# Kernel tuning notes

Hardware: AMD Instinct MI355X
Metric: run time of the kernel (lower is better)

The kernel has to match this reference:

```python
import jax, jax.numpy as jnp
import numpy as np

N = 50000      # nodes
E = 1600000    # edges (avg degree 32)
D = 64         # in_features
OUT = 64       # out_features


def setup_inputs() -> dict:
    key = jax.random.key(0)
    ks = jax.random.split(key, 6)
    x = jax.random.normal(ks[0], (N, D), jnp.float32)
    h0 = jax.random.normal(ks[1], (N, D), jnp.float32)
    edge_row = jax.random.randint(ks[2], (E,), 0, N, jnp.int32)
    edge_col = jax.random.randint(ks[3], (E,), 0, N, jnp.int32)
    edge_vals = jax.random.uniform(ks[4], (E,), jnp.float32)  # normalized adj values
    stdv = 1.0 / np.sqrt(OUT)
    W = jax.random.uniform(ks[5], (D, OUT), jnp.float32, -stdv, stdv)
    lamda = jnp.full((1,), 0.5, jnp.float32)
    s = jnp.full((1,), 0.1, jnp.float32)  # alpha in GCNII
    l = 4  # layer index
    return {"x": x, "h0": h0, "edge_vals": edge_vals, "W": W,
            "edge_row": edge_row, "edge_col": edge_col,
            "lamda": lamda, "s": s, "l": l}


def reference(x, h0, edge_vals, W, edge_row, edge_col, lamda, s, l):
    # theta = lamda / l
    theta = lamda / jnp.float32(l)  # [1]
    # hi = spmm(adj, x): COO gather-scale-scatter
    msgs = edge_vals[:, None] * x[edge_col]            # [E, D]
    hi = jax.ops.segment_sum(msgs, edge_row, num_segments=N)  # [N, D]
    # useAOR=True, variant=False: support = (1-s)*hi + s*h0; r = support
    support = (1.0 - s) * hi + s * h0                  # [N, D]
    # useDLR=True: output = theta * support @ W + (1-theta) * support
    output = theta * (support @ W) + (1.0 - theta) * support  # [N, OUT]
    # residual=False
    return output
```

## Files before the change

### kernel.cpp

```cpp
#include <hip/hip_runtime.h>

#define NN 50000
#define NE 1600000
#define DD 64
#define RB 128
#define NBK 391
#define BINS 512
#define EPB 4096
#define NBLKA 391
#define CAP 6144
#define G4 800000
#define CONVB 196

__device__ __forceinline__ unsigned f2bf(float f) {
    unsigned u = __float_as_uint(f);
    u += 0x7FFFu + ((u >> 16) & 1u);
    return (u >> 16) & 0xFFFFu;
}

__global__ __launch_bounds__(1024) void scatter_conv(
    const int* __restrict__ erow, const int* __restrict__ ecol,
    const float* __restrict__ evals, const float* __restrict__ x,
    uint2* __restrict__ xb, int* __restrict__ gcur,
    unsigned* __restrict__ pkv, unsigned char* __restrict__ rlb)
{
    int tid = threadIdx.x;
    if (blockIdx.x >= NBLKA) {
        int t = (blockIdx.x - NBLKA) * 1024 + tid;
        const float4* x4 = reinterpret_cast<const float4*>(x);
        #pragma unroll
        for (int i = 0; i < 4; ++i) {
            int g = i * (CONVB * 1024) + t;
            if (g < G4) {
                float4 v = x4[g];
                uint2 o;
                o.x = f2bf(v.x) | (f2bf(v.y) << 16);
                o.y = f2bf(v.z) | (f2bf(v.w) << 16);
                xb[g] = o;
            }
        }
        return;
    }

    __shared__ int hist[BINS];
    __shared__ int lstart[BINS];
    __shared__ int gbase[BINS];
    __shared__ unsigned datap[EPB];
    __shared__ unsigned char datarl[EPB];
    __shared__ unsigned short sbkt[EPB];

    if (tid < BINS) hist[tid] = 0;
    __syncthreads();

    int base = blockIdx.x * EPB;
    int r[4], c[4], bk[4]; float v[4];
    #pragma unroll
    for (int i = 0; i < 4; ++i) {
        int e = base + i * 1024 + tid;
        if (e < NE) {
            r[i] = erow[e]; c[i] = ecol[e]; v[i] = evals[e];
            bk[i] = r[i] >> 7;
            atomicAdd(&hist[bk[i]], 1);
        } else bk[i] = -1;
    }
    __syncthreads();

    if (tid < 64) {
        int cc[8], s = 0;
        #pragma unroll
        for (int i = 0; i < 8; ++i) { cc[i] = hist[tid * 8 + i]; s += cc[i]; }
        int vv = s;
        #pragma unroll
        for (int off = 1; off < 64; off <<= 1) {
            int u = __shfl_up(vv, off, 64);
            if (tid >= off) vv += u;
        }
        int run = vv - s;
        #pragma unroll
        for (int i = 0; i < 8; ++i) { lstart[tid * 8 + i] = run; run += cc[i]; }
    }
    __syncthreads();

    if (tid < BINS) {
        int cnt = hist[tid];
        gbase[tid] = cnt ? atomicAdd(&gcur[tid], cnt) : 0;
        hist[tid] = lstart[tid];
    }
    __syncthreads();

    #pragma unroll
    for (int i = 0; i < 4; ++i) {
        if (bk[i] >= 0) {
            int p = atomicAdd(&hist[bk[i]], 1);
            datap[p]  = (f2bf(v[i]) << 16) | (unsigned)c[i];
            datarl[p] = (unsigned char)(r[i] & (RB - 1));
            sbkt[p]   = (unsigned short)bk[i];
        }
    }
    __syncthreads();

    int total = NE - base; if (total > EPB) total = EPB;
    #pragma unroll
    for (int i = 0; i < 4; ++i) {
        int slot = i * 1024 + tid;
        if (slot < total) {
            int bb = sbkt[slot];
            int dst = bb * CAP + gbase[bb] + slot - lstart[bb];
            pkv[dst] = datap[slot];
            rlb[dst] = datarl[slot];
        }
    }
}

__global__ __launch_bounds__(1024) void row_sort(
    const int* __restrict__ gcur, unsigned* pkv,
    const unsigned char* __restrict__ rlb, int2* __restrict__ rs)
{
    __shared__ int rhist[RB];
    __shared__ int rstart[RB + 1];

    int tid = threadIdx.x;
    int b = blockIdx.x;
    int base = b * CAP;
    int count = gcur[b];

    if (tid < RB) rhist[tid] = 0;
    __syncthreads();

    unsigned av[CAP / 1024];
    int rl[CAP / 1024];
    #pragma unroll
    for (int i = 0; i < CAP / 1024; ++i) {
        int idx = i * 1024 + tid;
        if (idx < count) {
            av[i] = pkv[base + idx];
            rl[i] = rlb[base + idx];
            atomicAdd(&rhist[rl[i]], 1);
        } else rl[i] = -1;
    }
    __syncthreads();

    if (tid < 64) {
        int pc0 = (rhist[tid * 2] + 7) & ~7;
        int pc1 = (rhist[tid * 2 + 1] + 7) & ~7;
        int ssum = pc0 + pc1, vv = ssum;
        #pragma unroll
        for (int off = 1; off < 64; off <<= 1) {
            int u = __shfl_up(vv, off, 64);
            if (tid >= off) vv += u;
        }
        int run = vv - ssum;
        rstart[tid * 2]     = run;
        rstart[tid * 2 + 1] = run + pc0;
        if (tid == 63) rstart[RB] = run + pc0 + pc1;
    }
    __syncthreads();

    if (tid < RB) {
        int rr = b * RB + tid;
        if (rr < NN)
            rs[rr] = make_int2(base + rstart[tid], rstart[tid + 1] - rstart[tid]);
        rhist[tid] = rstart[tid];
    }
    __syncthreads();

    int p[CAP / 1024];
    #pragma unroll
    for (int i = 0; i < CAP / 1024; ++i)
        if (rl[i] >= 0) p[i] = atomicAdd(&rhist[rl[i]], 1);
    __syncthreads();

    #pragma unroll
    for (int i = 0; i < CAP / 1024; ++i)
        if (rl[i] >= 0) pkv[base + p[i]] = av[i];
    if (tid < RB)
        for (int idx = rhist[tid]; idx < rstart[tid + 1]; ++idx)
            pkv[base + idx] = 0;
}

__global__ __launch_bounds__(256, 4) void spmm_gemm(
    const uint2* __restrict__ xb, const float* __restrict__ h0,
    const float* __restrict__ W,  const float* __restrict__ lamda,
    const float* __restrict__ s_ptr, const int* __restrict__ l_ptr,
    const int2* __restrict__ rs, const unsigned* __restrict__ pkv,
    float* __restrict__ out)
{
    __shared__ float Wp[DD * DD];

    float theta = lamda[0] / (float)l_ptr[0];
    float s     = s_ptr[0];

    for (int i = threadIdx.x; i < DD * DD; i += 256) {
        int k = i >> 6, j = i & 63;
        float wv = theta * W[i];
        if (k == j) wv += (1.0f - theta);
        Wp[i] = wv;
    }
    __syncthreads();

    int tid    = threadIdx.x;
    int f4     = tid & 15;
    int parity = (tid >> 4) & 1;
    int gb     = tid & 48;
    int r      = blockIdx.x * 8 + (tid >> 5);

    int2 se = rs[r];
    int end = se.x + se.y;

    float4 acc = make_float4(0.f, 0.f, 0.f, 0.f);

    #define FMA1(U, Q)                                                      \
        {                                                                   \
            float vv = __uint_as_float((U) & 0xFFFF0000u);                  \
            acc.x = fmaf(vv, __uint_as_float((Q).x << 16), acc.x);          \
            acc.y = fmaf(vv, __uint_as_float((Q).x & 0xFFFF0000u), acc.y);  \
            acc.z = fmaf(vv, __uint_as_float((Q).y << 16), acc.z);          \
            acc.w = fmaf(vv, __uint_as_float((Q).y & 0xFFFF0000u), acc.w);  \
        }

    int e = se.x + parity * 8;
    unsigned myu = (e < end) ? pkv[e + (f4 & 7)] : 0;
    for (; e < end; e += 16) {
        unsigned nxt = (e + 16 < end) ? pkv[e + 16 + (f4 & 7)] : 0;
        unsigned u[8]; uint2 q[8];
        #pragma unroll
        for (int j = 0; j < 8; ++j) u[j] = __shfl(myu, gb + j, 64);
        #pragma unroll
        for (int j = 0; j < 8; ++j)
            q[j] = xb[(size_t)(u[j] & 0xFFFFu) * 16 + f4];
        #pragma unroll
        for (int j = 0; j < 8; ++j) FMA1(u[j], q[j]);
        myu = nxt;
    }
    #undef FMA1

    acc.x += __shfl_xor(acc.x, 16, 64);
    acc.y += __shfl_xor(acc.y, 16, 64);
    acc.z += __shfl_xor(acc.z, 16, 64);
    acc.w += __shfl_xor(acc.w, 16, 64);

    float4 hb = *reinterpret_cast<const float4*>(h0 + (size_t)r * DD + f4 * 4);
    float oms = 1.0f - s;
    float4 sup;
    sup.x = oms * acc.x + s * hb.x;
    sup.y = oms * acc.y + s * hb.y;
    sup.z = oms * acc.z + s * hb.z;
    sup.w = oms * acc.w + s * hb.w;

    float4 o = make_float4(0.f, 0.f, 0.f, 0.f);
    #pragma unroll
    for (int kk = 0; kk < 32; ++kk) {
        int k = parity * 32 + kk;
        float comp = ((kk & 3) == 0) ? sup.x :
                     ((kk & 3) == 1) ? sup.y :
                     ((kk & 3) == 2) ? sup.z : sup.w;
        float sk = __shfl(comp, gb + parity * 8 + (kk >> 2), 64);
        float4 w = *reinterpret_cast<const float4*>(&Wp[k * DD + f4 * 4]);
        o.x = fmaf(sk, w.x, o.x);
        o.y = fmaf(sk, w.y, o.y);
        o.z = fmaf(sk, w.z, o.z);
        o.w = fmaf(sk, w.w, o.w);
    }
    o.x += __shfl_xor(o.x, 16, 64);
    o.y += __shfl_xor(o.y, 16, 64);
    o.z += __shfl_xor(o.z, 16, 64);
    o.w += __shfl_xor(o.w, 16, 64);

    if (parity == 0)
        *reinterpret_cast<float4*>(out + (size_t)r * DD + f4 * 4) = o;
}

extern "C" void kernel_launch(void* const* d_in, const int* in_sizes, int n_in,
                              void* d_out, int out_size, void* d_ws, size_t ws_size,
                              hipStream_t stream) {
    const float* x     = (const float*)d_in[0];
    const float* h0    = (const float*)d_in[1];
    const float* evals = (const float*)d_in[2];
    const float* W     = (const float*)d_in[3];
    const int*   erow  = (const int*)d_in[4];
    const int*   ecol  = (const int*)d_in[5];
    const float* lamda = (const float*)d_in[6];
    const float* s_ptr = (const float*)d_in[7];
    const int*   l_ptr = (const int*)d_in[8];
    float* out = (float*)d_out;

    char* ws = (char*)d_ws;
    int*           gcur = (int*)ws;
    int2*          rs   = (int2*)(ws + 2048);
    size_t         pkv_off = 2048 + (((size_t)NN * 8 + 255) & ~(size_t)255);
    unsigned*      pkv  = (unsigned*)(ws + pkv_off);
    uint2*         xb   = (uint2*)(ws + pkv_off + (size_t)NBK * CAP * 4);
    unsigned char* rlb  = (unsigned char*)(ws + pkv_off + (size_t)NBK * CAP * 4
                                              + (size_t)NN * DD * 2);

    hipMemsetAsync(gcur, 0, 2048, stream);

    scatter_conv<<<NBLKA + CONVB, 1024, 0, stream>>>(erow, ecol, evals, x, xb,
                                                     gcur, pkv, rlb);
    row_sort    <<<NBK, 1024, 0, stream>>>(gcur, pkv, rlb, rs);
    spmm_gemm   <<<NN / 8, 256, 0, stream>>>(xb, h0, W, lamda, s_ptr, l_ptr,
                                             rs, pkv, out);
}
```

Baseline: 72.24 us.

## Fuse row-bucket sort into SpMM+GEMM kernel using shared-memory sorted edges

Merges the row_sort and spmm_gemm kernels into one. Each block sorts a 64-row bucket's edges into shared memory and then computes the SpMM and the dense transform for those rows directly from LDS. Bucket size shrinks from 128 to 64 rows (782 buckets, capacity 3072), and the scatter histogram widens to 1024 bins. This removes the global write-back of sorted edges, the rs array and one kernel launch. The cost is only 782 blocks of 512 threads, each holding about 28KB of LDS and the W staging, so occupancy and load balance may suffer. The xb base is now byte-offset by NBK*CAP*5 = 12,011,520 bytes, which is 8-byte aligned.

After: 68.09 us, median of 2. 5.7% less time.

```diff
diff --git a/kernel.cpp b/kernel.cpp
--- a/kernel.cpp
+++ b/kernel.cpp
@@ -3,12 +3,12 @@
 #define NN 50000
 #define NE 1600000
 #define DD 64
-#define RB 128
-#define NBK 391
-#define BINS 512
+#define RB 64
+#define NBK 782
+#define BINS 1024
 #define EPB 4096
 #define NBLKA 391
-#define CAP 6144
+#define CAP 3072
 #define G4 800000
 #define CONVB 196
 
@@ -59,16 +59,16 @@
         int e = base + i * 1024 + tid;
         if (e < NE) {
             r[i] = erow[e]; c[i] = ecol[e]; v[i] = evals[e];
-            bk[i] = r[i] >> 7;
+            bk[i] = r[i] >> 6;
             atomicAdd(&hist[bk[i]], 1);
         } else bk[i] = -1;
     }
     __syncthreads();
 
     if (tid < 64) {
-        int cc[8], s = 0;
-        #pragma unroll
-        for (int i = 0; i < 8; ++i) { cc[i] = hist[tid * 8 + i]; s += cc[i]; }
+        int cc[16], s = 0;
+        #pragma unroll
+        for (int i = 0; i < 16; ++i) { cc[i] = hist[tid * 16 + i]; s += cc[i]; }
         int vv = s;
         #pragma unroll
         for (int off = 1; off < 64; off <<= 1) {
@@ -77,7 +77,7 @@
         }
         int run = vv - s;
         #pragma unroll
-        for (int i = 0; i < 8; ++i) { lstart[tid * 8 + i] = run; run += cc[i]; }
+        for (int i = 0; i < 16; ++i) { lstart[tid * 16 + i] = run; run += cc[i]; }
     }
     __syncthreads();
 
@@ -112,10 +112,16 @@
     }
 }
 
-__global__ __launch_bounds__(1024) void row_sort(
-    const int* __restrict__ gcur, unsigned* pkv,
-    const unsigned char* __restrict__ rlb, int2* __restrict__ rs)
+__global__ __launch_bounds__(512) void sort_spmm_gemm(
+    const int* __restrict__ gcur, const unsigned* __restrict__ pkv,
+    const unsigned char* __restrict__ rlb,
+    const uint2* __restrict__ xb, const float* __restrict__ h0,
+    const float* __restrict__ W,  const float* __restrict__ lamda,
+    const float* __restrict__ s_ptr, const int* __restrict__ l_ptr,
+    float* __restrict__ out)
 {
+    __shared__ unsigned pkbuf[CAP];
+    __shared__ float Wp[DD * DD];
     __shared__ int rhist[RB];
     __shared__ int rstart[RB + 1];
 
@@ -124,14 +130,24 @@
     int base = b * CAP;
     int count = gcur[b];
 
+    float theta = lamda[0] / (float)l_ptr[0];
+    float s     = s_ptr[0];
+    float oms   = 1.0f - s;
+
+    for (int i = tid; i < DD * DD; i += 512) {
+        int k = i >> 6, j = i & 63;
+        float wv = theta * W[i];
+        if (k == j) wv += (1.0f - theta);
+        Wp[i] = wv;
+    }
     if (tid < RB) rhist[tid] = 0;
     __syncthreads();
 
-    unsigned av[CAP / 1024];
-    int rl[CAP / 1024];
-    #pragma unroll
-    for (int i = 0; i < CAP / 1024; ++i) {
-        int idx = i * 1024 + tid;
+    unsigned av[CAP / 512];
+    int rl[CAP / 512];
+    #pragma unroll
+    for (int i = 0; i < CAP / 512; ++i) {
+        int idx = i * 512 + tid;
         if (idx < count) {
             av[i] = pkv[base + idx];
             rl[i] = rlb[base + idx];
@@ -141,73 +157,36 @@
     __syncthreads();
 
     if (tid < 64) {
-        int pc0 = (rhist[tid * 2] + 7) & ~7;
-        int pc1 = (rhist[tid * 2 + 1] + 7) & ~7;
-        int ssum = pc0 + pc1, vv = ssum;
+        int pc = (rhist[tid] + 7) & ~7;
+        int vv = pc;
         #pragma unroll
         for (int off = 1; off < 64; off <<= 1) {
             int u = __shfl_up(vv, off, 64);
             if (tid >= off) vv += u;
         }
-        int run = vv - ssum;
-        rstart[tid * 2]     = run;
-        rstart[tid * 2 + 1] = run + pc0;
-        if (tid == 63) rstart[RB] = run + pc0 + pc1;
-    }
-    __syncthreads();
-
-    if (tid < RB) {
-        int rr = b * RB + tid;
-        if (rr < NN)
-            rs[rr] = make_int2(base + rstart[tid], rstart[tid + 1] - rstart[tid]);
-        rhist[tid] = rstart[tid];
-    }
-    __syncthreads();
-
-    int p[CAP / 1024];
-    #pragma unroll
-    for (int i = 0; i < CAP / 1024; ++i)
-        if (rl[i] >= 0) p[i] = atomicAdd(&rhist[rl[i]], 1);
-    __syncthreads();
-
-    #pragma unroll
-    for (int i = 0; i < CAP / 1024; ++i)
-        if (rl[i] >= 0) pkv[base + p[i]] = av[i];
+        rstart[tid] = vv - pc;
+        if (tid == 63) rstart[RB] = vv;
+    }
+    __syncthreads();
+    if (tid < RB) rhist[tid] = rstart[tid];
+    __syncthreads();
+
+    #pragma unroll
+    for (int i = 0; i < CAP / 512; ++i)
+        if (rl[i] >= 0) {
+            int p = atomicAdd(&rhist[rl[i]], 1);
+            pkbuf[p] = av[i];
+        }
+    __syncthreads();
     if (tid < RB)
         for (int idx = rhist[tid]; idx < rstart[tid + 1]; ++idx)
-            pkv[base + idx] = 0;
-}
-
-__global__ __launch_bounds__(256, 4) void spmm_gemm(
-    const uint2* __restrict__ xb, const float* __restrict__ h0,
-    const float* __restrict__ W,  const float* __restrict__ lamda,
-    const float* __restrict__ s_ptr, const int* __restrict__ l_ptr,
-    const int2* __restrict__ rs, const unsigned* __restrict__ pkv,
-    float* __restrict__ out)
-{
-    __shared__ float Wp[DD * DD];
-
-    float theta = lamda[0] / (float)l_ptr[0];
-    float s     = s_ptr[0];
-
-    for (int i = threadIdx.x; i < DD * DD; i += 256) {
-        int k = i >> 6, j = i & 63;
-        float wv = theta * W[i];
-        if (k == j) wv += (1.0f - theta);
-        Wp[i] = wv;
-    }
-    __syncthreads();
-
-    int tid    = threadIdx.x;
+            pkbuf[idx] = 0;
+    __syncthreads();
+
     int f4     = tid & 15;
     int parity = (tid >> 4) & 1;
     int gb     = tid & 48;
-    int r      = blockIdx.x * 8 + (tid >> 5);
-
-    int2 se = rs[r];
-    int end = se.x + se.y;
-
-    float4 acc = make_float4(0.f, 0.f, 0.f, 0.f);
+    int slot   = tid >> 5;
 
     #define FMA1(U, Q)                                                      \
         {                                                                   \
@@ -218,56 +197,66 @@
             acc.w = fmaf(vv, __uint_as_float((Q).y & 0xFFFF0000u), acc.w);  \
         }
 
-    int e = se.x + parity * 8;
-    unsigned myu = (e < end) ? pkv[e + (f4 & 7)] : 0;
-    for (; e < end; e += 16) {
-        unsigned nxt = (e + 16 < end) ? pkv[e + 16 + (f4 & 7)] : 0;
-        unsigned u[8]; uint2 q[8];
-        #pragma unroll
-        for (int j = 0; j < 8; ++j) u[j] = __shfl(myu, gb + j, 64);
-        #pragma unroll
-        for (int j = 0; j < 8; ++j)
-            q[j] = xb[(size_t)(u[j] & 0xFFFFu) * 16 + f4];
-        #pragma unroll
-        for (int j = 0; j < 8; ++j) FMA1(u[j], q[j]);
-        myu = nxt;
+    #pragma unroll
+    for (int pass = 0; pass < 4; ++pass) {
+        int rr = pass * 16 + slot;
+        int r  = b * RB + rr;
+        if (r < NN) {
+            int e0  = rstart[rr];
+            int end = rstart[rr + 1];
+
+            float4 acc = make_float4(0.f, 0.f, 0.f, 0.f);
+            for (int e = e0 + parity * 8; e < end; e += 16) {
+                uint4 ua = *reinterpret_cast<const uint4*>(&pkbuf[e]);
+                uint4 ub = *reinterpret_cast<const uint4*>(&pkbuf[e + 4]);
+                uint2 q0 = xb[(size_t)(ua.x & 0xFFFFu) * 16 + f4];
+                uint2 q1 = xb[(size_t)(ua.y & 0xFFFFu) * 16 + f4];
+                uint2 q2 = xb[(size_t)(ua.z & 0xFFFFu) * 16 + f4];
+                uint2 q3 = xb[(size_t)(ua.w & 0xFFFFu) * 16 + f4];
+                uint2 q4 = xb[(size_t)(ub.x & 0xFFFFu) * 16 + f4];
+                uint2 q5 = xb[(size_t)(ub.y & 0xFFFFu) * 16 + f4];
+                uint2 q6 = xb[(size_t)(ub.z & 0xFFFFu) * 16 + f4];
+                uint2 q7 = xb[(size_t)(ub.w & 0xFFFFu) * 16 + f4];
+                FMA1(ua.x, q0); FMA1(ua.y, q1); FMA1(ua.z, q2); FMA1(ua.w, q3);
+                FMA1(ub.x, q4); FMA1(ub.y, q5); FMA1(ub.z, q6); FMA1(ub.w, q7);
+            }
+
+            acc.x += __shfl_xor(acc.x, 16, 64);
+            acc.y += __shfl_xor(acc.y, 16, 64);
+            acc.z += __shfl_xor(acc.z, 16, 64);
+            acc.w += __shfl_xor(acc.w, 16, 64);
+
+            float4 hb = *reinterpret_cast<const float4*>(h0 + (size_t)r * DD + f4 * 4);
+            float4 sup;
+            sup.x = oms * acc.x + s * hb.x;
+            sup.y = oms * acc.y + s * hb.y;
+            sup.z = oms * acc.z + s * hb.z;
+            sup.w = oms * acc.w + s * hb.w;
+
+            float4 o = make_float4(0.f, 0.f, 0.f, 0.f);
+            #pragma unroll
+            for (int kk = 0; kk < 32; ++kk) {
+                int k = parity * 32 + kk;
+                float comp = ((kk & 3) == 0) ? sup.x :
+                             ((kk & 3) == 1) ? sup.y :
+                             ((kk & 3) == 2) ? sup.z : sup.w;
+                float sk = __shfl(comp, gb + parity * 8 + (kk >> 2), 64);
+                float4 w = *reinterpret_cast<const float4*>(&Wp[k * DD + f4 * 4]);
+                o.x = fmaf(sk, w.x, o.x);
+                o.y = fmaf(sk, w.y, o.y);
+                o.z = fmaf(sk, w.z, o.z);
+                o.w = fmaf(sk, w.w, o.w);
+            }
+            o.x += __shfl_xor(o.x, 16, 64);
+            o.y += __shfl_xor(o.y, 16, 64);
+            o.z += __shfl_xor(o.z, 16, 64);
+            o.w += __shfl_xor(o.w, 16, 64);
+
+            if (parity == 0)
+                *reinterpret_cast<float4*>(out + (size_t)r * DD + f4 * 4) = o;
+        }
     }
     #undef FMA1
-
-    acc.x += __shfl_xor(acc.x, 16, 64);
-    acc.y += __shfl_xor(acc.y, 16, 64);
-    acc.z += __shfl_xor(acc.z, 16, 64);
-    acc.w += __shfl_xor(acc.w, 16, 64);
-
-    float4 hb = *reinterpret_cast<const float4*>(h0 + (size_t)r * DD + f4 * 4);
-    float oms = 1.0f - s;
-    float4 sup;
-    sup.x = oms * acc.x + s * hb.x;
-    sup.y = oms * acc.y + s * hb.y;
-    sup.z = oms * acc.z + s * hb.z;
-    sup.w = oms * acc.w + s * hb.w;
-
-    float4 o = make_float4(0.f, 0.f, 0.f, 0.f);
-    #pragma unroll
-    for (int kk = 0; kk < 32; ++kk) {
-        int k = parity * 32 + kk;
-        float comp = ((kk & 3) == 0) ? sup.x :
-                     ((kk & 3) == 1) ? sup.y :
-                     ((kk & 3) == 2) ? sup.z : sup.w;
-        float sk = __shfl(comp, gb + parity * 8 + (kk >> 2), 64);
-        float4 w = *reinterpret_cast<const float4*>(&Wp[k * DD + f4 * 4]);
-        o.x = fmaf(sk, w.x, o.x);
-        o.y = fmaf(sk, w.y, o.y);
-        o.z = fmaf(sk, w.z, o.z);
-        o.w = fmaf(sk, w.w, o.w);
-    }
-    o.x += __shfl_xor(o.x, 16, 64);
-    o.y += __shfl_xor(o.y, 16, 64);
-    o.z += __shfl_xor(o.z, 16, 64);
-    o.w += __shfl_xor(o.w, 16, 64);
-
-    if (parity == 0)
-        *reinterpret_cast<float4*>(out + (size_t)r * DD + f4 * 4) = o;
 }
 
 extern "C" void kernel_launch(void* const* d_in, const int* in_sizes, int n_in,
@@ -286,18 +275,14 @@
 
     char* ws = (char*)d_ws;
     int*           gcur = (int*)ws;
-    int2*          rs   = (int2*)(ws + 2048);
-    size_t         pkv_off = 2048 + (((size_t)NN * 8 + 255) & ~(size_t)255);
-    unsigned*      pkv  = (unsigned*)(ws + pkv_off);
-    uint2*         xb   = (uint2*)(ws + pkv_off + (size_t)NBK * CAP * 4);
-    unsigned char* rlb  = (unsigned char*)(ws + pkv_off + (size_t)NBK * CAP * 4
-                                              + (size_t)NN * DD * 2);
-
-    hipMemsetAsync(gcur, 0, 2048, stream);
-
-    scatter_conv<<<NBLKA + CONVB, 1024, 0, stream>>>(erow, ecol, evals, x, xb,
-                                                     gcur, pkv, rlb);
-    row_sort    <<<NBK, 1024, 0, stream>>>(gcur, pkv, rlb, rs);
-    spmm_gemm   <<<NN / 8, 256, 0, stream>>>(xb, h0, W, lamda, s_ptr, l_ptr,
-                                             rs, pkv, out);
-}
+    unsigned*      pkv  = (unsigned*)(ws + 4096);
+    unsigned char* rlb  = (unsigned char*)(ws + 4096 + (size_t)NBK * CAP * 4);
+    uint2*         xb   = (uint2*)(ws + 4096 + (size_t)NBK * CAP * 5);
+
+    hipMemsetAsync(gcur, 0, 4096, stream);
+
+    scatter_conv  <<<NBLKA + CONVB, 1024, 0, stream>>>(erow, ecol, evals, x, xb,
+                                                       gcur, pkv, rlb);
+    sort_spmm_gemm<<<NBK, 512, 0, stream>>>(gcur, pkv, rlb, xb, h0, W,
+                                            lamda, s_ptr, l_ptr, out);
+}
```
